# Performance work log

Hardware: AMD Instinct MI355X
Metric: run time of the kernel (lower is better)

## Reference

```python
import jax, jax.numpy as jnp
import numpy as np

D = 1024
H = 16
HD = D // H
FF = 4 * D
EPS = 1e-5


def _layernorm(x, g, s):
    m = x.mean(-1, keepdims=True)
    v = ((x - m) ** 2).mean(-1, keepdims=True)  # unbiased=False
    return g * (x - m) / jnp.sqrt(v + EPS) + s


def _gelu_tanh(x):
    c = jnp.sqrt(2.0 / jnp.pi).astype(x.dtype)
    return 0.5 * x * (1 + jnp.tanh(c * (x + 0.044715 * x ** 3)))


def setup_inputs() -> dict:
    key = jax.random.key(0)
    ks = jax.random.split(key, 12)
    B, T = 2, 2048
    std = 0.02
    x = jax.random.normal(ks[0], (B, T, D), jnp.float32)
    wq = jax.random.normal(ks[1], (D, D), jnp.float32) * std
    wk = jax.random.normal(ks[2], (D, D), jnp.float32) * std
    wv = jax.random.normal(ks[3], (D, D), jnp.float32) * std
    wo = jax.random.normal(ks[4], (D, D), jnp.float32) * std
    bo = jnp.zeros((D,), jnp.float32)
    w1 = jax.random.normal(ks[5], (FF, D), jnp.float32) * std
    b1 = jnp.zeros((FF,), jnp.float32)
    w2 = jax.random.normal(ks[6], (D, FF), jnp.float32) * std
    b2 = jnp.zeros((D,), jnp.float32)
    g1 = jnp.ones((D,), jnp.float32)
    s1 = jnp.zeros((D,), jnp.float32)
    g2 = jnp.ones((D,), jnp.float32)
    s2 = jnp.zeros((D,), jnp.float32)
    return {"x": x, "wq": wq, "wk": wk, "wv": wv, "wo": wo, "bo": bo,
            "w1": w1, "b1": b1, "w2": w2, "b2": b2,
            "g1": g1, "s1": s1, "g2": g2, "s2": s2}


def reference(x, wq, wk, wv, wo, bo, w1, b1, w2, b2, g1, s1, g2, s2):
    B, T, _ = x.shape
    # pre-LN attention
    h = _layernorm(x, g1, s1)
    q = (h @ wq.T).reshape(B, T, H, HD).transpose(0, 2, 1, 3)  # [B,H,T,HD]
    k = (h @ wk.T).reshape(B, T, H, HD).transpose(0, 2, 1, 3)
    v = (h @ wv.T).reshape(B, T, H, HD).transpose(0, 2, 1, 3)
    scores = jnp.einsum('bhqd,bhkd->bhqk', q, k)
    causal = jnp.triu(jnp.ones((T, T), bool), k=1)
    scores = jnp.where(causal, -jnp.inf, scores)
    attn = jax.nn.softmax(scores / jnp.sqrt(jnp.float32(HD)), axis=-1)
    ctx = jnp.einsum('bhqk,bhkd->bhqd', attn, v)
    ctx = ctx.transpose(0, 2, 1, 3).reshape(B, T, D)
    x = x + (ctx @ wo.T + bo)
    # pre-LN MLP
    h2 = _layernorm(x, g2, s2)
    ff = _gelu_tanh(h2 @ w1.T + b1) @ w2.T + b2
    return x + ff
```

## Files before the change

kernel.cpp:

```cpp
#include <hip/hip_runtime.h>
#include <hip/hip_bf16.h>
#include <stdint.h>


typedef __attribute__((ext_vector_type(8))) __bf16 bf16x8;
typedef __attribute__((ext_vector_type(4))) __bf16 bf16x4;
typedef __attribute__((ext_vector_type(4))) float  f32x4;

#define DD    1024
#define TSEQ  2048
#define NTOK  4096
#define FFD   4096

#define ASM_VMCNT4() asm volatile("s_waitcnt vmcnt(4)" ::: "memory")
#define ASM_VMCNT0() asm volatile("s_waitcnt vmcnt(0)" ::: "memory")
#define ASM_LGKM0()  asm volatile("s_waitcnt lgkmcnt(0)" ::: "memory")

__device__ __forceinline__ void gll16(const void* g, void* l) {
  __builtin_amdgcn_global_load_lds(
      (const __attribute__((address_space(1))) unsigned int*)g,
      (__attribute__((address_space(3))) unsigned int*)l, 16, 0, 0);
}

__device__ __forceinline__ float gelu_f(float v) {
  float u = 0.7978845608028654f * (v + 0.044715f * v * v * v);
  float t = 1.0f - 2.0f / (1.0f + __expf(2.0f * u));
  return 0.5f * v * (1.0f + t);
}

__global__ __launch_bounds__(256) void cvt_weights(
    const float* __restrict__ wq, const float* __restrict__ wk,
    const float* __restrict__ wv, const float* __restrict__ wo,
    const float* __restrict__ w1, const float* __restrict__ w2,
    __bf16* __restrict__ dst)
{
  size_t i4 = (size_t)blockIdx.x * 256 + threadIdx.x;
  size_t e = i4 * 4;
  const float* src; size_t off;
  if (e < (size_t)4 * 1048576) {
    int sel = (int)(e >> 20);
    src = sel == 0 ? wq : sel == 1 ? wk : sel == 2 ? wv : wo;
    off = e & 1048575;
  } else if (e < (size_t)8 * 1048576) {
    src = w1; off = e - (size_t)4 * 1048576;
  } else {
    src = w2; off = e - (size_t)8 * 1048576;
  }
  float4 v = *(const float4*)(src + off);
  bf16x4 o;
  o[0] = (__bf16)v.x; o[1] = (__bf16)v.y; o[2] = (__bf16)v.z; o[3] = (__bf16)v.w;
  *(bf16x4*)(dst + e) = o;
}

__global__ __launch_bounds__(256) void ln_kernel(
    const float* __restrict__ x, const float* __restrict__ gw,
    const float* __restrict__ sw, __bf16* __restrict__ out)
{
  const int row  = blockIdx.x * 4 + (threadIdx.x >> 6);
  const int lane = threadIdx.x & 63;
  const float4* xr = (const float4*)(x + (size_t)row * DD);
  float4 v[4];
  float s = 0.f, sq = 0.f;
#pragma unroll
  for (int i = 0; i < 4; ++i) {
    v[i] = xr[i * 64 + lane];
    s  += v[i].x + v[i].y + v[i].z + v[i].w;
    sq += v[i].x * v[i].x + v[i].y * v[i].y + v[i].z * v[i].z + v[i].w * v[i].w;
  }
#pragma unroll
  for (int off = 32; off >= 1; off >>= 1) {
    s  += __shfl_xor(s, off);
    sq += __shfl_xor(sq, off);
  }
  const float mean = s * (1.f / DD);
  const float rstd = rsqrtf(sq * (1.f / DD) - mean * mean + 1e-5f);
  const float4* gr = (const float4*)gw;
  const float4* sr = (const float4*)sw;
#pragma unroll
  for (int i = 0; i < 4; ++i) {
    float4 gv = gr[i * 64 + lane];
    float4 sv = sr[i * 64 + lane];
    bf16x4 o;
    o[0] = (__bf16)(gv.x * (v[i].x - mean) * rstd + sv.x);
    o[1] = (__bf16)(gv.y * (v[i].y - mean) * rstd + sv.y);
    o[2] = (__bf16)(gv.z * (v[i].z - mean) * rstd + sv.z);
    o[3] = (__bf16)(gv.w * (v[i].w - mean) * rstd + sv.w);
    *(bf16x4*)&out[(size_t)row * DD + (size_t)(i * 64 + lane) * 4] = o;
  }
}

template<int MODE>
__global__ __launch_bounds__(512, 2)
void gemm256(const __bf16* __restrict__ A, int lda,
             const __bf16* __restrict__ Bw, int ldb,
             __bf16* __restrict__ Cout, const float* __restrict__ bias,
             __bf16* __restrict__ voutT, int M, int N, int K)
{
  __shared__ __bf16 sm[65536];
  const int t = threadIdx.x;
  const int lane = t & 63;
  const int l15 = lane & 15, g = lane >> 4;
  const int w = t >> 6;
  const int wm = w >> 2, wn = w & 3;
  const int m0 = blockIdx.y * 256, n0 = blockIdx.x * 256;

  if (MODE == 2) {
    const int kz = blockIdx.z;
    A    += (size_t)kz * 1024;
    Bw   += (size_t)kz * 1024;
    Cout += (size_t)kz * (size_t)M * N;
  }

  auto STAGE_A = [&](int kt, int h, int b) {
#pragma unroll
    for (int i = 0; i < 2; ++i) {
      const int slot = i * 512 + t;
      const int row  = h * 128 + (slot >> 3);
      const int gc   = (slot & 7) ^ (row & 7);
      gll16(A + (size_t)(m0 + row) * lda + kt * 64 + gc * 8,
            sm + b * 32768 + h * 8192 + slot * 8);
    }
  };
  auto STAGE_B = [&](int kt, int h, int b) {
#pragma unroll
    for (int i = 0; i < 2; ++i) {
      const int slot = i * 512 + t;
      const int row  = h * 128 + (slot >> 3);
      const int gc   = (slot & 7) ^ (row & 7);
      gll16(Bw + (size_t)(n0 + row) * ldb + kt * 64 + gc * 8,
            sm + b * 32768 + 16384 + h * 8192 + slot * 8);
    }
  };

  f32x4 acc[8][4] = {};
  const int NT = K >> 6;

  STAGE_A(0, 0, 0); STAGE_A(0, 1, 0);
  STAGE_B(0, 0, 0); STAGE_B(0, 1, 0);
  STAGE_B(1, 0, 1); STAGE_B(1, 1, 1);
  ASM_VMCNT4();
  __builtin_amdgcn_s_barrier();

  for (int kt = 0; kt < NT; ++kt) {
    const int cb = kt & 1;
    const __bf16* sA = sm + cb * 32768;
    const __bf16* sB = sm + cb * 32768 + 16384;
    const bool pf1 = (kt + 1 < NT);
    const bool pf2 = (kt + 2 < NT);

    bf16x8 afl[4][2], afh[4][2], bfl[2][2], bfh[2][2];

#pragma unroll
    for (int mi = 0; mi < 4; ++mi) {
      const int row = wm * 128 + mi * 16 + l15;
#pragma unroll
      for (int ks = 0; ks < 2; ++ks)
        afl[mi][ks] = *(const bf16x8*)&sA[row * 64 + (((ks * 4 + g) ^ (row & 7)) * 8)];
    }
#pragma unroll
    for (int ni = 0; ni < 2; ++ni) {
      const int row = wn * 64 + ni * 16 + l15;
#pragma unroll
      for (int ks = 0; ks < 2; ++ks)
        bfl[ni][ks] = *(const bf16x8*)&sB[row * 64 + (((ks * 4 + g) ^ (row & 7)) * 8)];
    }
    if (pf1) STAGE_A(kt + 1, 0, cb ^ 1);
    __builtin_amdgcn_s_barrier();
    ASM_LGKM0();
    __builtin_amdgcn_sched_barrier(0);
    __builtin_amdgcn_s_setprio(1);
#pragma unroll
    for (int ks = 0; ks < 2; ++ks)
#pragma unroll
      for (int mi = 0; mi < 4; ++mi)
#pragma unroll
        for (int ni = 0; ni < 2; ++ni)
          acc[mi][ni] = __builtin_amdgcn_mfma_f32_16x16x32_bf16(
              afl[mi][ks], bfl[ni][ks], acc[mi][ni], 0, 0, 0);
    __builtin_amdgcn_s_setprio(0);
    __builtin_amdgcn_s_barrier();

#pragma unroll
    for (int ni = 0; ni < 2; ++ni) {
      const int row = wn * 64 + (ni + 2) * 16 + l15;
#pragma unroll
      for (int ks = 0; ks < 2; ++ks)
        bfh[ni][ks] = *(const bf16x8*)&sB[row * 64 + (((ks * 4 + g) ^ (row & 7)) * 8)];
    }
    if (pf1) STAGE_A(kt + 1, 1, cb ^ 1);
    __builtin_amdgcn_s_barrier();
    ASM_LGKM0();
    __builtin_amdgcn_sched_barrier(0);
    __builtin_amdgcn_s_setprio(1);
#pragma unroll
    for (int ks = 0; ks < 2; ++ks)
#pragma unroll
      for (int mi = 0; mi < 4; ++mi)
#pragma unroll
        for (int ni = 0; ni < 2; ++ni)
          acc[mi][ni + 2] = __builtin_amdgcn_mfma_f32_16x16x32_bf16(
              afl[mi][ks], bfh[ni][ks], acc[mi][ni + 2], 0, 0, 0);
    __builtin_amdgcn_s_setprio(0);
    __builtin_amdgcn_s_barrier();

#pragma unroll
    for (int mi = 0; mi < 4; ++mi) {
      const int row = wm * 128 + (mi + 4) * 16 + l15;
#pragma unroll
      for (int ks = 0; ks < 2; ++ks)
        afh[mi][ks] = *(const bf16x8*)&sA[row * 64 + (((ks * 4 + g) ^ (row & 7)) * 8)];
    }
    if (pf2) STAGE_B(kt + 2, 0, cb);
    __builtin_amdgcn_s_barrier();
    ASM_LGKM0();
    __builtin_amdgcn_sched_barrier(0);
    __builtin_amdgcn_s_setprio(1);
#pragma unroll
    for (int ks = 0; ks < 2; ++ks)
#pragma unroll
      for (int mi = 0; mi < 4; ++mi)
#pragma unroll
        for (int ni = 0; ni < 2; ++ni)
          acc[mi + 4][ni + 2] = __builtin_amdgcn_mfma_f32_16x16x32_bf16(
              afh[mi][ks], bfh[ni][ks], acc[mi + 4][ni + 2], 0, 0, 0);
    __builtin_amdgcn_s_setprio(0);
    __builtin_amdgcn_s_barrier();

    if (pf2) STAGE_B(kt + 2, 1, cb);
    __builtin_amdgcn_s_barrier();
    __builtin_amdgcn_s_setprio(1);
#pragma unroll
    for (int ks = 0; ks < 2; ++ks)
#pragma unroll
      for (int mi = 0; mi < 4; ++mi)
#pragma unroll
        for (int ni = 0; ni < 2; ++ni)
          acc[mi + 4][ni] = __builtin_amdgcn_mfma_f32_16x16x32_bf16(
              afh[mi][ks], bfl[ni][ks], acc[mi + 4][ni], 0, 0, 0);
    __builtin_amdgcn_s_setprio(0);
    if (pf1) { if (pf2) ASM_VMCNT4(); else ASM_VMCNT0(); }
    __builtin_amdgcn_s_barrier();
  }

#pragma unroll
  for (int mi = 0; mi < 8; ++mi) {
    const int rr0 = m0 + wm * 128 + mi * 16 + 4 * g;
#pragma unroll
    for (int ni = 0; ni < 4; ++ni) {
      const int cc = n0 + wn * 64 + ni * 16 + l15;
      if (MODE == 0 && n0 + wn * 64 >= 2048) {
        const int b  = rr0 >> 11;
        const int t0 = rr0 & 2047;
        const int vc = cc - 2048;
        const int h = vc >> 6, d = vc & 63;
        bf16x4 o;
        o[0] = (__bf16)acc[mi][ni][0]; o[1] = (__bf16)acc[mi][ni][1];
        o[2] = (__bf16)acc[mi][ni][2]; o[3] = (__bf16)acc[mi][ni][3];
        *(bf16x4*)&voutT[(((size_t)(b * 16 + h)) * 64 + d) * 2048 + t0] = o;
      } else {
        const int ldc = (MODE == 0) ? 2048 : N;
#pragma unroll
        for (int r = 0; r < 4; ++r) {
          float v = acc[mi][ni][r];
          if (MODE == 0 && cc < 1024) v *= 0.125f;
          if (MODE == 1) { v += bias[cc]; v = gelu_f(v); }
          Cout[(size_t)(rr0 + r) * ldc + cc] = (__bf16)v;
        }
      }
    }
  }
}

__global__ __launch_bounds__(256) void ff2_reduce(
    const __bf16* __restrict__ part, const float* __restrict__ x2,
    const float* __restrict__ b2, float* __restrict__ out)
{
  const size_t e = ((size_t)blockIdx.x * 256 + threadIdx.x) * 4;
  float4 r = *(const float4*)(x2 + e);
  const float4 b = *(const float4*)(b2 + (e & 1023));
  r.x += b.x; r.y += b.y; r.z += b.z; r.w += b.w;
#pragma unroll
  for (int s = 0; s < 4; ++s) {
    bf16x4 p = *(const bf16x4*)(part + (size_t)s * 4194304 + e);
    r.x += (float)p[0]; r.y += (float)p[1]; r.z += (float)p[2]; r.w += (float)p[3];
  }
  *(float4*)(out + e) = r;
}

template<bool BIAS, bool RES>
__global__ __launch_bounds__(256, 3)
void gemm_bt(const __bf16* __restrict__ A, const __bf16* __restrict__ Bw,
             float* __restrict__ Cout, const float* __restrict__ bias,
             const float* __restrict__ res, int M, int N, int K)
{
  __shared__ __bf16 As[128 * 64];
  __shared__ __bf16 Bs[128 * 64];
  const int t    = threadIdx.x;
  const int lane = t & 63;
  const int l15  = lane & 15;
  const int g    = lane >> 4;
  const int w    = t >> 6;
  const int wr   = w >> 1, wc = w & 1;
  const int m0 = blockIdx.y * 128;
  const int n0 = blockIdx.x * 128;
  const int srow = t >> 3;
  const int scol = (t & 7) * 8;

  f32x4 acc[4][4] = {};
  const __bf16* Ap = A  + (size_t)m0 * K;
  const __bf16* Bp = Bw + (size_t)n0 * K;

  for (int k0 = 0; k0 < K; k0 += 64) {
#pragma unroll
    for (int i = 0; i < 4; ++i) {
      const int row = i * 32 + srow;
      gll16(Ap + (size_t)row * K + k0 + scol, &As[row * 64 + scol]);
    }
#pragma unroll
    for (int i = 0; i < 4; ++i) {
      const int row = i * 32 + srow;
      gll16(Bp + (size_t)row * K + k0 + scol, &Bs[row * 64 + scol]);
    }
    __syncthreads();
#pragma unroll
    for (int ks = 0; ks < 2; ++ks) {
      bf16x8 af[4], bfr[4];
#pragma unroll
      for (int mi = 0; mi < 4; ++mi)
        af[mi] = *(const bf16x8*)&As[(wr * 64 + mi * 16 + l15) * 64 + ks * 32 + g * 8];
#pragma unroll
      for (int ni = 0; ni < 4; ++ni)
        bfr[ni] = *(const bf16x8*)&Bs[(wc * 64 + ni * 16 + l15) * 64 + ks * 32 + g * 8];
#pragma unroll
      for (int mi = 0; mi < 4; ++mi)
#pragma unroll
        for (int ni = 0; ni < 4; ++ni)
          acc[mi][ni] = __builtin_amdgcn_mfma_f32_16x16x32_bf16(af[mi], bfr[ni], acc[mi][ni], 0, 0, 0);
    }
    __syncthreads();
  }

  const int crow0 = m0 + wr * 64;
  const int ccol0 = n0 + wc * 64;
#pragma unroll
  for (int mi = 0; mi < 4; ++mi) {
#pragma unroll
    for (int r = 0; r < 4; ++r) {
      const int rr = crow0 + mi * 16 + 4 * g + r;
#pragma unroll
      for (int ni = 0; ni < 4; ++ni) {
        const int cc = ccol0 + ni * 16 + l15;
        float v = acc[mi][ni][r];
        if (BIAS) v += bias[cc];
        if (RES)  v += res[(size_t)rr * N + cc];
        Cout[(size_t)rr * N + cc] = v;
      }
    }
  }
}

__global__ __launch_bounds__(256, 2)
void attn_kernel(const __bf16* __restrict__ qk, const __bf16* __restrict__ vT,
                 __bf16* __restrict__ ctx)
{
  __shared__ __bf16 Ks[64 * 64];
  __shared__ __bf16 VTs[64 * 64];
  __shared__ __bf16 Ps[4][16 * 64];
  const int t    = threadIdx.x;
  const int lane = t & 63;
  const int l15  = lane & 15;
  const int g    = lane >> 4;
  const int w    = t >> 6;
  const int qt = gridDim.x - 1 - blockIdx.x;
  const int hh = blockIdx.y;
  const int bb = blockIdx.z;
  const int q0 = qt * 64;

  const int qrow = q0 + w * 16 + l15;
  const size_t qkrow = ((size_t)(bb * 2048 + qrow)) * 2048 + hh * 64;
  bf16x8 qf0 = *(const bf16x8*)&qk[qkrow + g * 8];
  bf16x8 qf1 = *(const bf16x8*)&qk[qkrow + 32 + g * 8];

  const int kk = t >> 2;
  const int c0 = (t & 3) * 16;
  const __bf16* kbase = &qk[((size_t)(bb * 2048) + kk) * 2048 + 1024 + hh * 64 + c0];
  const __bf16* vbase = &vT[(((size_t)(bb * 16 + hh)) * 64 + kk) * 2048 + c0];
  const int xw  = (kk & 7) << 4;
  char* kdst = (char*)Ks  + kk * 128;
  char* vdst = (char*)VTs + kk * 128;
  const int cw0 = ((((t & 3) * 2)    ) << 4) ^ xw;
  const int cw1 = ((((t & 3) * 2) + 1) << 4) ^ xw;

  f32x4 acc[4] = {};
  float mrun = -1e30f, lrun = 0.f;

  bf16x8 ka0, ka1, va0, va1, kb0, kb1, vb0, vb1;

  auto LOAD = [&](int kt, bf16x8& k0, bf16x8& k1, bf16x8& v0, bf16x8& v1) {
    const __bf16* kp = kbase + (size_t)kt * 64 * 2048;
    k0 = *(const bf16x8*)(kp);
    k1 = *(const bf16x8*)(kp + 8);
    const __bf16* vp = vbase + kt * 64;
    v0 = *(const bf16x8*)(vp);
    v1 = *(const bf16x8*)(vp + 8);
  };
  auto WRITE = [&](bf16x8& k0, bf16x8& k1, bf16x8& v0, bf16x8& v1) {
    *(bf16x8*)(kdst + cw0) = k0;
    *(bf16x8*)(kdst + cw1) = k1;
    *(bf16x8*)(vdst + cw0) = v0;
    *(bf16x8*)(vdst + cw1) = v1;
  };

  const int xr = (l15 & 7) << 4;
  char* pw = (char*)Ps[w] + l15 * 128;

  auto COMPUTE = [&](int kt) {
    f32x4 s[4];
#pragma unroll
    for (int f = 0; f < 4; ++f) {
      const char* kb = (const char*)Ks + (f * 16 + l15) * 128;
      bf16x8 a0 = *(const bf16x8*)(kb + ((g << 4) ^ xr));
      bf16x8 a1 = *(const bf16x8*)(kb + (((4 + g) << 4) ^ xr));
      f32x4 z = {};
      z = __builtin_amdgcn_mfma_f32_16x16x32_bf16(a0, qf0, z, 0, 0, 0);
      z = __builtin_amdgcn_mfma_f32_16x16x32_bf16(a1, qf1, z, 0, 0, 0);
      s[f] = z;
    }

    float pmax = -1e30f;
    if (kt == qt) {
      const int qg = q0 + w * 16 + l15;
#pragma unroll
      for (int f = 0; f < 4; ++f)
#pragma unroll
        for (int r = 0; r < 4; ++r) {
          const int kg = kt * 64 + f * 16 + g * 4 + r;
          if (kg > qg) s[f][r] = -1e30f;
          pmax = fmaxf(pmax, s[f][r]);
        }
    } else {
#pragma unroll
      for (int f = 0; f < 4; ++f)
#pragma unroll
        for (int r = 0; r < 4; ++r) pmax = fmaxf(pmax, s[f][r]);
    }
    pmax = fmaxf(pmax, __shfl_xor(pmax, 16));
    pmax = fmaxf(pmax, __shfl_xor(pmax, 32));

    if (__any(pmax > mrun)) {
      const float mnew  = fmaxf(mrun, pmax);
      const float alpha = __expf(mrun - mnew);
      float al[4];
#pragma unroll
      for (int r = 0; r < 4; ++r) al[r] = __shfl(alpha, g * 4 + r);
#pragma unroll
      for (int nf = 0; nf < 4; ++nf)
#pragma unroll
        for (int r = 0; r < 4; ++r) acc[nf][r] *= al[r];
      lrun *= alpha;
      mrun = mnew;
    }

    float lsum = 0.f;
#pragma unroll
    for (int f = 0; f < 4; ++f)
#pragma unroll
      for (int r = 0; r < 4; ++r) {
        float p = __expf(s[f][r] - mrun);
        s[f][r] = p;
        lsum += p;
      }
    lsum += __shfl_xor(lsum, 16);
    lsum += __shfl_xor(lsum, 32);
    lrun += lsum;

#pragma unroll
    for (int f = 0; f < 4; ++f) {
      bf16x4 pk;
      pk[0] = (__bf16)s[f][0]; pk[1] = (__bf16)s[f][1];
      pk[2] = (__bf16)s[f][2]; pk[3] = (__bf16)s[f][3];
      *(bf16x4*)(pw + ((((f * 2 + (g >> 1)) << 4) ^ xr) + (g & 1) * 8)) = pk;
    }
    asm volatile("s_waitcnt lgkmcnt(0)" ::: "memory");

#pragma unroll
    for (int ks = 0; ks < 2; ++ks) {
      bf16x8 pa = *(const bf16x8*)(pw + (((ks * 4 + g) << 4) ^ xr));
#pragma unroll
      for (int nf = 0; nf < 4; ++nf) {
        const char* vb = (const char*)VTs + (nf * 16 + l15) * 128;
        bf16x8 vf = *(const bf16x8*)(vb + (((ks * 4 + g) << 4) ^ xr));
        acc[nf] = __builtin_amdgcn_mfma_f32_16x16x32_bf16(pa, vf, acc[nf], 0, 0, 0);
      }
    }
  };

  LOAD(0, ka0, ka1, va0, va1);
  int kt = 0;
  for (;;) {
    ASM_VMCNT0();
    __syncthreads();
    WRITE(ka0, ka1, va0, va1);
    if (kt < qt) LOAD(kt + 1, kb0, kb1, vb0, vb1);
    __syncthreads();
    COMPUTE(kt);
    if (++kt > qt) break;

    ASM_VMCNT0();
    __syncthreads();
    WRITE(kb0, kb1, vb0, vb1);
    if (kt < qt) LOAD(kt + 1, ka0, ka1, va0, va1);
    __syncthreads();
    COMPUTE(kt);
    if (++kt > qt) break;
  }

  float li[4];
#pragma unroll
  for (int r = 0; r < 4; ++r) li[r] = 1.0f / __shfl(lrun, g * 4 + r);
#pragma unroll
  for (int nf = 0; nf < 4; ++nf)
#pragma unroll
    for (int r = 0; r < 4; ++r) {
      const int row = q0 + w * 16 + 4 * g + r;
      ctx[((size_t)(bb * 2048 + row)) * DD + hh * 64 + nf * 16 + l15] =
          (__bf16)(acc[nf][r] * li[r]);
    }
}

extern "C" void kernel_launch(void* const* d_in, const int* in_sizes, int n_in,
                              void* d_out, int out_size, void* d_ws, size_t ws_size,
                              hipStream_t stream)
{
  (void)in_sizes; (void)n_in; (void)out_size; (void)ws_size;
  const float* x  = (const float*)d_in[0];
  const float* wq = (const float*)d_in[1];
  const float* wk = (const float*)d_in[2];
  const float* wv = (const float*)d_in[3];
  const float* wo = (const float*)d_in[4];
  const float* bo = (const float*)d_in[5];
  const float* w1 = (const float*)d_in[6];
  const float* b1 = (const float*)d_in[7];
  const float* w2 = (const float*)d_in[8];
  const float* b2 = (const float*)d_in[9];
  const float* g1 = (const float*)d_in[10];
  const float* s1 = (const float*)d_in[11];
  const float* g2 = (const float*)d_in[12];
  const float* s2 = (const float*)d_in[13];
  float* out = (float*)d_out;

  char* ws = (char*)d_ws;
  __bf16* wbf  = (__bf16*)ws;
  __bf16* hbuf = (__bf16*)(ws + 25165824);
  __bf16* qkb  = (__bf16*)(ws + 33554432);
  __bf16* vbT  = (__bf16*)(ws + 50331648);
  __bf16* ctxb = (__bf16*)(ws + 58720256);
  float*  x2   = (float*)(ws + 67108864);
  __bf16* ffb  = (__bf16*)(ws + 83886080);
  __bf16* part = (__bf16*)(ws + 33554432);

  cvt_weights<<<12288, 256, 0, stream>>>(wq, wk, wv, wo, w1, w2, wbf);
  ln_kernel<<<1024, 256, 0, stream>>>(x, g1, s1, hbuf);

  gemm256<0><<<dim3(12, 16), 512, 0, stream>>>(
      hbuf, 1024, wbf, 1024, qkb, nullptr, vbT, NTOK, 3072, 1024);

  dim3 ga(32, 16, 2);
  attn_kernel<<<ga, 256, 0, stream>>>(qkb, vbT, ctxb);

  gemm_bt<true, true><<<dim3(8, 32), 256, 0, stream>>>(
      ctxb, wbf + 3145728, x2, bo, x, NTOK, DD, DD);
  ln_kernel<<<1024, 256, 0, stream>>>(x2, g2, s2, hbuf);

  gemm256<1><<<dim3(16, 16), 512, 0, stream>>>(
      hbuf, 1024, wbf + 4194304, 1024, ffb, b1, nullptr, NTOK, FFD, 1024);

  gemm256<2><<<dim3(4, 16, 4), 512, 0, stream>>>(
      ffb, 4096, wbf + 8388608, 4096, part, nullptr, nullptr, NTOK, DD, 1024);
  ff2_reduce<<<4096, 256, 0, stream>>>(part, x2, b2, out);
}
```

Before: 241.8 us.

## Replace phased ping-pong GEMM pipeline with simple whole-tile double buffering

The GEMM main loop previously split each k-step into four MFMA phases. Each phase interleaved half-tile LDS fragment reads, half-tile global-to-LDS prefetches (A one step ahead, B two steps ahead), explicit vmcnt/lgkmcnt waits, s_setprio and many barriers. It now issues the full next A and B tile prefetch at the top of each iteration and loads all fragments at once. It then runs all 64 MFMAs and ends with a single __syncthreads. Precomputed base offsets cut address arithmetic and barrier count. The cost is coarser overlap between memory and compute, no priority hints, and more live fragment registers.

```diff
diff --git a/kernel.cpp b/kernel.cpp
--- a/kernel.cpp
+++ b/kernel.cpp
@@ -12,9 +12,7 @@
 #define NTOK  4096
 #define FFD   4096
 
-#define ASM_VMCNT4() asm volatile("s_waitcnt vmcnt(4)" ::: "memory")
 #define ASM_VMCNT0() asm volatile("s_waitcnt vmcnt(0)" ::: "memory")
-#define ASM_LGKM0()  asm volatile("s_waitcnt lgkmcnt(0)" ::: "memory")
 
 __device__ __forceinline__ void gll16(const void* g, void* l) {
   __builtin_amdgcn_global_load_lds(
@@ -111,135 +109,65 @@
     Cout += (size_t)kz * (size_t)M * N;
   }
 
-  auto STAGE_A = [&](int kt, int h, int b) {
-#pragma unroll
-    for (int i = 0; i < 2; ++i) {
-      const int slot = i * 512 + t;
-      const int row  = h * 128 + (slot >> 3);
-      const int gc   = (slot & 7) ^ (row & 7);
-      gll16(A + (size_t)(m0 + row) * lda + kt * 64 + gc * 8,
-            sm + b * 32768 + h * 8192 + slot * 8);
-    }
+  const int srow = t >> 3;
+  const int schunk = t & 7;
+  const int gc = schunk ^ (srow & 7);
+  const __bf16* gA = A  + (size_t)(m0 + srow) * lda + gc * 8;
+  const __bf16* gB = Bw + (size_t)(n0 + srow) * ldb + gc * 8;
+  char* smb = (char*)sm;
+  const int sdst = t * 16;
+
+  auto STAGE = [&](int kt, int cur) {
+    char* dA = smb + cur * 65536;
+    char* dB = dA + 32768;
+    const __bf16* a = gA + kt * 64;
+    const __bf16* b = gB + kt * 64;
+#pragma unroll
+    for (int i = 0; i < 4; ++i)
+      gll16(a + (size_t)i * 64 * lda, dA + i * 8192 + sdst);
+#pragma unroll
+    for (int i = 0; i < 4; ++i)
+      gll16(b + (size_t)i * 64 * ldb, dB + i * 8192 + sdst);
   };
-  auto STAGE_B = [&](int kt, int h, int b) {
-#pragma unroll
-    for (int i = 0; i < 2; ++i) {
-      const int slot = i * 512 + t;
-      const int row  = h * 128 + (slot >> 3);
-      const int gc   = (slot & 7) ^ (row & 7);
-      gll16(Bw + (size_t)(n0 + row) * ldb + kt * 64 + gc * 8,
-            sm + b * 32768 + 16384 + h * 8192 + slot * 8);
-    }
-  };
+
+  const int xa = l15 & 7;
+  const int baseA0 = (wm * 128 + l15) * 128 + ((g ^ xa) << 4);
+  const int baseA1 = (wm * 128 + l15) * 128 + (((4 + g) ^ xa) << 4);
+  const int baseB0 = 32768 + (wn * 64 + l15) * 128 + ((g ^ xa) << 4);
+  const int baseB1 = 32768 + (wn * 64 + l15) * 128 + (((4 + g) ^ xa) << 4);
 
   f32x4 acc[8][4] = {};
   const int NT = K >> 6;
 
-  STAGE_A(0, 0, 0); STAGE_A(0, 1, 0);
-  STAGE_B(0, 0, 0); STAGE_B(0, 1, 0);
-  STAGE_B(1, 0, 1); STAGE_B(1, 1, 1);
-  ASM_VMCNT4();
-  __builtin_amdgcn_s_barrier();
+  STAGE(0, 0);
+  __syncthreads();
 
   for (int kt = 0; kt < NT; ++kt) {
-    const int cb = kt & 1;
-    const __bf16* sA = sm + cb * 32768;
-    const __bf16* sB = sm + cb * 32768 + 16384;
-    const bool pf1 = (kt + 1 < NT);
-    const bool pf2 = (kt + 2 < NT);
-
-    bf16x8 afl[4][2], afh[4][2], bfl[2][2], bfh[2][2];
-
-#pragma unroll
-    for (int mi = 0; mi < 4; ++mi) {
-      const int row = wm * 128 + mi * 16 + l15;
-#pragma unroll
-      for (int ks = 0; ks < 2; ++ks)
-        afl[mi][ks] = *(const bf16x8*)&sA[row * 64 + (((ks * 4 + g) ^ (row & 7)) * 8)];
-    }
-#pragma unroll
-    for (int ni = 0; ni < 2; ++ni) {
-      const int row = wn * 64 + ni * 16 + l15;
-#pragma unroll
-      for (int ks = 0; ks < 2; ++ks)
-        bfl[ni][ks] = *(const bf16x8*)&sB[row * 64 + (((ks * 4 + g) ^ (row & 7)) * 8)];
-    }
-    if (pf1) STAGE_A(kt + 1, 0, cb ^ 1);
-    __builtin_amdgcn_s_barrier();
-    ASM_LGKM0();
-    __builtin_amdgcn_sched_barrier(0);
-    __builtin_amdgcn_s_setprio(1);
+    const int cur = kt & 1;
+    if (kt + 1 < NT) STAGE(kt + 1, cur ^ 1);
+
+    const char* bufb = smb + cur * 65536;
+    bf16x8 af[8][2], bfr[4][2];
+#pragma unroll
+    for (int mi = 0; mi < 8; ++mi) {
+      af[mi][0] = *(const bf16x8*)(bufb + baseA0 + mi * 2048);
+      af[mi][1] = *(const bf16x8*)(bufb + baseA1 + mi * 2048);
+    }
+#pragma unroll
+    for (int ni = 0; ni < 4; ++ni) {
+      bfr[ni][0] = *(const bf16x8*)(bufb + baseB0 + ni * 2048);
+      bfr[ni][1] = *(const bf16x8*)(bufb + baseB1 + ni * 2048);
+    }
 #pragma unroll
     for (int ks = 0; ks < 2; ++ks)
 #pragma unroll
-      for (int mi = 0; mi < 4; ++mi)
-#pragma unroll
-        for (int ni = 0; ni < 2; ++ni)
+      for (int mi = 0; mi < 8; ++mi)
+#pragma unroll
+        for (int ni = 0; ni < 4; ++ni)
           acc[mi][ni] = __builtin_amdgcn_mfma_f32_16x16x32_bf16(
-              afl[mi][ks], bfl[ni][ks], acc[mi][ni], 0, 0, 0);
-    __builtin_amdgcn_s_setprio(0);
-    __builtin_amdgcn_s_barrier();
-
-#pragma unroll
-    for (int ni = 0; ni < 2; ++ni) {
-      const int row = wn * 64 + (ni + 2) * 16 + l15;
-#pragma unroll
-      for (int ks = 0; ks < 2; ++ks)
-        bfh[ni][ks] = *(const bf16x8*)&sB[row * 64 + (((ks * 4 + g) ^ (row & 7)) * 8)];
-    }
-    if (pf1) STAGE_A(kt + 1, 1, cb ^ 1);
-    __builtin_amdgcn_s_barrier();
-    ASM_LGKM0();
-    __builtin_amdgcn_sched_barrier(0);
-    __builtin_amdgcn_s_setprio(1);
-#pragma unroll
-    for (int ks = 0; ks < 2; ++ks)
-#pragma unroll
-      for (int mi = 0; mi < 4; ++mi)
-#pragma unroll
-        for (int ni = 0; ni < 2; ++ni)
-          acc[mi][ni + 2] = __builtin_amdgcn_mfma_f32_16x16x32_bf16(
-              afl[mi][ks], bfh[ni][ks], acc[mi][ni + 2], 0, 0, 0);
-    __builtin_amdgcn_s_setprio(0);
-    __builtin_amdgcn_s_barrier();
-
-#pragma unroll
-    for (int mi = 0; mi < 4; ++mi) {
-      const int row = wm * 128 + (mi + 4) * 16 + l15;
-#pragma unroll
-      for (int ks = 0; ks < 2; ++ks)
-        afh[mi][ks] = *(const bf16x8*)&sA[row * 64 + (((ks * 4 + g) ^ (row & 7)) * 8)];
-    }
-    if (pf2) STAGE_B(kt + 2, 0, cb);
-    __builtin_amdgcn_s_barrier();
-    ASM_LGKM0();
-    __builtin_amdgcn_sched_barrier(0);
-    __builtin_amdgcn_s_setprio(1);
-#pragma unroll
-    for (int ks = 0; ks < 2; ++ks)
-#pragma unroll
-      for (int mi = 0; mi < 4; ++mi)
-#pragma unroll
-        for (int ni = 0; ni < 2; ++ni)
-          acc[mi + 4][ni + 2] = __builtin_amdgcn_mfma_f32_16x16x32_bf16(
-              afh[mi][ks], bfh[ni][ks], acc[mi + 4][ni + 2], 0, 0, 0);
-    __builtin_amdgcn_s_setprio(0);
-    __builtin_amdgcn_s_barrier();
-
-    if (pf2) STAGE_B(kt + 2, 1, cb);
-    __builtin_amdgcn_s_barrier();
-    __builtin_amdgcn_s_setprio(1);
-#pragma unroll
-    for (int ks = 0; ks < 2; ++ks)
-#pragma unroll
-      for (int mi = 0; mi < 4; ++mi)
-#pragma unroll
-        for (int ni = 0; ni < 2; ++ni)
-          acc[mi + 4][ni] = __builtin_amdgcn_mfma_f32_16x16x32_bf16(
-              afh[mi][ks], bfl[ni][ks], acc[mi + 4][ni], 0, 0, 0);
-    __builtin_amdgcn_s_setprio(0);
-    if (pf1) { if (pf2) ASM_VMCNT4(); else ASM_VMCNT0(); }
-    __builtin_amdgcn_s_barrier();
+              af[mi][ks], bfr[ni][ks], acc[mi][ni], 0, 0, 0);
+
+    __syncthreads();
   }
 
 #pragma unroll
```

Result: faster. 237.1 us (-2.0%).
